# Kernel optimization log

Hardware: AMD Instinct MI355X
Metric: run time of the kernel (lower is better)

Reference implementation:

```python
import jax, jax.numpy as jnp
import numpy as np

N_LAYERS = 4
HID = 64
N_NODES = 50000
N_EDGES = 800000
N_GRAPHS = 256
NUM_ATOM = 100
NUM_BOND = 4
BN_EPS = 1e-5
GATE_EPS = 1e-6


def _batch_norm(x, gamma, beta):
    # training-mode BatchNorm1d over the node/edge dimension
    mu = jnp.mean(x, axis=0)
    var = jnp.var(x, axis=0)
    return gamma * (x - mu) * jax.lax.rsqrt(var + BN_EPS) + beta


def setup_inputs() -> dict:
    key = jax.random.key(0)
    ks = jax.random.split(key, 12)
    h = jax.random.randint(ks[0], (N_NODES,), 0, NUM_ATOM)
    e = jax.random.randint(ks[1], (N_EDGES,), 0, NUM_BOND)
    src = jax.random.randint(ks[2], (N_EDGES,), 0, N_NODES)
    dst = jax.random.randint(ks[3], (N_EDGES,), 0, N_NODES)
    graph_ids = jnp.sort(jax.random.randint(ks[4], (N_NODES,), 0, N_GRAPHS))
    node_emb = jax.random.normal(ks[5], (NUM_ATOM, HID), dtype=jnp.float32) * 0.1
    edge_emb = jax.random.normal(ks[6], (NUM_BOND, HID), dtype=jnp.float32) * 0.1
    bn_h_gamma = jnp.ones((N_LAYERS, HID), jnp.float32)
    bn_h_beta = jnp.zeros((N_LAYERS, HID), jnp.float32)
    bn_e_gamma = jnp.ones((N_LAYERS, HID), jnp.float32)
    bn_e_beta = jnp.zeros((N_LAYERS, HID), jnp.float32)
    W1 = jax.random.normal(ks[7], (HID, HID // 2), dtype=jnp.float32) * (1.0 / np.sqrt(HID))
    b1 = jnp.zeros((HID // 2,), jnp.float32)
    W2 = jax.random.normal(ks[8], (HID // 2, HID // 4), dtype=jnp.float32) * (1.0 / np.sqrt(HID // 2))
    b2 = jnp.zeros((HID // 4,), jnp.float32)
    W3 = jax.random.normal(ks[9], (HID // 4, 1), dtype=jnp.float32) * (1.0 / np.sqrt(HID // 4))
    b3 = jnp.zeros((1,), jnp.float32)
    return {"h": h, "e": e, "src": src, "dst": dst, "graph_ids": graph_ids,
            "node_emb": node_emb, "edge_emb": edge_emb,
            "bn_h_gamma": bn_h_gamma, "bn_h_beta": bn_h_beta,
            "bn_e_gamma": bn_e_gamma, "bn_e_beta": bn_e_beta,
            "W1": W1, "b1": b1, "W2": W2, "b2": b2, "W3": W3, "b3": b3}


def reference(h, e, src, dst, graph_ids, node_emb, edge_emb,
              bn_h_gamma, bn_h_beta, bn_e_gamma, bn_e_beta,
              W1, b1, W2, b2, W3, b3):
    hf = node_emb[h]          # [N, HID] node encoder
    ef = edge_emb[e]          # [E, HID] edge encoder
    ones_e = jnp.ones((N_EDGES,), hf.dtype)
    deg = jax.ops.segment_sum(ones_e, dst, num_segments=N_NODES)
    norm = jax.lax.rsqrt(jnp.maximum(deg, 1.0))[:, None]  # deg^-0.5, clamp(min=1)
    for l in range(N_LAYERS):
        h_in, e_in = hf, ef
        e_new = hf[src] + hf[dst] + ef            # gather: edge gate pre-activation
        sigma = jax.nn.sigmoid(e_new)
        hn = hf * norm
        msg = jax.ops.segment_sum(sigma * hn[src], dst, num_segments=N_NODES)
        den = jax.ops.segment_sum(sigma, dst, num_segments=N_NODES)
        h_new = (hn + msg / (den + GATE_EPS)) * norm
        h_new = _batch_norm(h_new, bn_h_gamma[l], bn_h_beta[l])
        e_new = _batch_norm(e_new, bn_e_gamma[l], bn_e_beta[l])
        hf = h_in + jax.nn.relu(h_new)            # residual
        ef = e_in + jax.nn.relu(e_new)
    # per-graph mean pooling (dgl.mean_nodes over the batched graph)
    ones_n = jnp.ones((N_NODES,), hf.dtype)
    counts = jax.ops.segment_sum(ones_n, graph_ids, num_segments=N_GRAPHS)
    hg = jax.ops.segment_sum(hf, graph_ids, num_segments=N_GRAPHS)
    hg = hg / jnp.maximum(counts, 1.0)[:, None]   # [G, HID]
    x = jax.nn.relu(hg @ W1 + b1)
    x = jax.nn.relu(x @ W2 + b2)
    return x @ W3 + b3                            # [G, 1]
```

## Files before the change

### kernel.cpp

```cpp
#include <hip/hip_runtime.h>
#include <math.h>

#define N_NODES 50000
#define N_EDGES 800000
#define HID 64
#define N_GRAPHS 256
#define BN_EPS 1e-5f
#define GATE_EPS 1e-6f

static inline size_t align256(size_t x) { return (x + 255) & ~(size_t)255; }


__global__ void k_zero(int* __restrict__ p, int n) {
    for (int i = blockIdx.x * blockDim.x + threadIdx.x; i < n; i += gridDim.x * blockDim.x)
        p[i] = 0;
}

__global__ void k_deg(const int* __restrict__ dst, int* __restrict__ deg) {
    for (int i = blockIdx.x * blockDim.x + threadIdx.x; i < N_EDGES; i += gridDim.x * blockDim.x)
        atomicAdd(&deg[dst[i]], 1);
}

__global__ void k_norm(const int* __restrict__ deg, float* __restrict__ norm) {
    int i = blockIdx.x * blockDim.x + threadIdx.x;
    if (i < N_NODES) norm[i] = 1.0f / sqrtf(fmaxf((float)deg[i], 1.0f));
}

__global__ void k_scan1(const int* __restrict__ deg, int* __restrict__ start,
                        int* __restrict__ blksum) {
    __shared__ int s[256];
    int t = threadIdx.x;
    int i = blockIdx.x * 256 + t;
    int v = (i < N_NODES) ? deg[i] : 0;
    s[t] = v;
    __syncthreads();
    for (int off = 1; off < 256; off <<= 1) {
        int x = (t >= off) ? s[t - off] : 0;
        __syncthreads();
        s[t] += x;
        __syncthreads();
    }
    if (i < N_NODES) start[i] = s[t] - v;
    if (t == 255) blksum[blockIdx.x] = s[255];
}

__global__ void k_scan2(int* __restrict__ blksum, int nb) {
    __shared__ int s[256];
    int t = threadIdx.x;
    int v = (t < nb) ? blksum[t] : 0;
    s[t] = v;
    __syncthreads();
    for (int off = 1; off < 256; off <<= 1) {
        int x = (t >= off) ? s[t - off] : 0;
        __syncthreads();
        s[t] += x;
        __syncthreads();
    }
    if (t < nb) blksum[t] = s[t] - v;
}

__global__ void k_scan3(int* __restrict__ start, const int* __restrict__ blksum,
                        int* __restrict__ cursor) {
    int i = blockIdx.x * 256 + threadIdx.x;
    if (i < N_NODES) {
        int v = start[i] + blksum[blockIdx.x];
        start[i] = v;
        cursor[i] = v;
    }
    if (blockIdx.x == 0 && threadIdx.x == 0) start[N_NODES] = N_EDGES;
}

__global__ void k_scatter(const int* __restrict__ dst, const int* __restrict__ src,
                          const int* __restrict__ etype, const float* __restrict__ norm,
                          int* __restrict__ cursor,
                          int* __restrict__ edge_pack, float* __restrict__ edge_norm) {
    for (int i = blockIdx.x * blockDim.x + threadIdx.x; i < N_EDGES; i += gridDim.x * blockDim.x) {
        int p = atomicAdd(&cursor[dst[i]], 1);
        int s = src[i];
        edge_pack[p] = s | (etype[i] << 24);
        edge_norm[p] = norm[s];
    }
}

__global__ __launch_bounds__(256) void k_embed(const int* __restrict__ h,
                                               const float* __restrict__ node_emb,
                                               float4* __restrict__ hf4) {
    const int total4 = N_NODES * (HID / 4);
    for (int i = blockIdx.x * blockDim.x + threadIdx.x; i < total4; i += gridDim.x * blockDim.x) {
        int n = i >> 4, c4 = i & 15;
        hf4[i] = ((const float4*)node_emb)[h[n] * (HID / 4) + c4];
    }
}

template <int MODE>
__global__ __launch_bounds__(256) void k_edge(
    const int* __restrict__ start, const int* __restrict__ edge_pack,
    const float* __restrict__ edge_norm, const float* __restrict__ edge_emb,
    float* __restrict__ ef,
    const float* __restrict__ hf_old, const float* __restrict__ hf_new,
    const float* __restrict__ norm, float* __restrict__ h_new,
    const float* __restrict__ stats_prev, const float* __restrict__ gamma_prev,
    const float* __restrict__ beta_prev,
    float* __restrict__ stats_e_out, float* __restrict__ stats_h_out) {
    const int lane = threadIdx.x & 63;
    const int gw = blockIdx.x * (blockDim.x >> 6) + (threadIdx.x >> 6);
    const int nw = gridDim.x * (blockDim.x >> 6);

    __shared__ float s_emb[4 * HID];
    if (MODE <= 1) {
        for (int i = threadIdx.x; i < 4 * HID; i += blockDim.x) s_emb[i] = edge_emb[i];
        __syncthreads();
    }
    float a_prev = 0.f, c_prev = 0.f;
    if (MODE >= 1) {
        float s1 = stats_prev[lane], s2 = stats_prev[HID + lane];
        float mu = s1 * (1.0f / N_EDGES);
        float var = s2 * (1.0f / N_EDGES) - mu * mu;
        float rstd = 1.0f / sqrtf(var + BN_EPS);
        a_prev = gamma_prev[lane] * rstd;
        c_prev = beta_prev[lane] - mu * a_prev;
    }

    float sum_e = 0.f, sumsq_e = 0.f, sum_h = 0.f, sumsq_h = 0.f;
    for (int n = gw; n < N_NODES; n += nw) {
        const int jbeg = start[n], jend = start[n + 1];
        const float h_new_n = hf_new[n * HID + lane];
        const float h_old_n = (MODE >= 1) ? hf_old[n * HID + lane] : 0.f;
        float amsg = 0.f, aden = 0.f;
        if (jbeg < jend) {
            int pk = edge_pack[jbeg];
            float ns = edge_norm[jbeg];
            int s = pk & 0xFFFFFF;
            float hs = hf_new[s * HID + lane];
            float ho = (MODE >= 1) ? hf_old[s * HID + lane] : 0.f;
            float efp = (MODE >= 2) ? ef[(size_t)jbeg * HID + lane] : 0.f;
            for (int j = jbeg; j < jend; ++j) {
                const int jn = (j + 1 < jend) ? j + 1 : jend - 1;
                const int pk_n = edge_pack[jn];
                const float ns_n = edge_norm[jn];
                const int s_n = pk_n & 0xFFFFFF;
                const float hs_n = hf_new[s_n * HID + lane];
                const float ho_n = (MODE >= 1) ? hf_old[s_n * HID + lane] : 0.f;
                const float efp_n = (MODE >= 2) ? ef[(size_t)jn * HID + lane] : 0.f;
                float efv;
                if (MODE == 0) {
                    efv = s_emb[(pk >> 24) * HID + lane];
                } else if (MODE == 1) {
                    const float ef0 = s_emb[(pk >> 24) * HID + lane];
                    const float ep = ho + h_old_n + ef0;
                    efv = ef0 + fmaxf(a_prev * ep + c_prev, 0.f);
                    ef[(size_t)j * HID + lane] = efv;
                } else {
                    const float ep = ho + h_old_n + efp;
                    efv = efp + fmaxf(a_prev * ep + c_prev, 0.f);
                    if (MODE == 2) ef[(size_t)j * HID + lane] = efv;
                }
                const float en = hs + h_new_n + efv;
                const float sg = 1.0f / (1.0f + __expf(-en));
                amsg += sg * hs * ns;
                aden += sg;
                if (MODE != 3) { sum_e += en; sumsq_e += en * en; }
                pk = pk_n; ns = ns_n; s = s_n; hs = hs_n; ho = ho_n; efp = efp_n;
            }
        }
        const float nm = norm[n];
        const float hval = (h_new_n * nm + amsg / (aden + GATE_EPS)) * nm;
        h_new[n * HID + lane] = hval;
        sum_h += hval;
        sumsq_h += hval * hval;
    }

    __shared__ float sred[4][256];
    sred[0][threadIdx.x] = sum_e;
    sred[1][threadIdx.x] = sumsq_e;
    sred[2][threadIdx.x] = sum_h;
    sred[3][threadIdx.x] = sumsq_h;
    __syncthreads();
    if (threadIdx.x < 64) {
        const int t = threadIdx.x;
        if (MODE != 3) {
            float t1 = sred[0][t] + sred[0][t + 64] + sred[0][t + 128] + sred[0][t + 192];
            float t2 = sred[1][t] + sred[1][t + 64] + sred[1][t + 128] + sred[1][t + 192];
            atomicAdd(&stats_e_out[t], t1);
            atomicAdd(&stats_e_out[HID + t], t2);
        }
        float t3 = sred[2][t] + sred[2][t + 64] + sred[2][t + 128] + sred[2][t + 192];
        float t4 = sred[3][t] + sred[3][t + 64] + sred[3][t + 128] + sred[3][t + 192];
        atomicAdd(&stats_h_out[t], t3);
        atomicAdd(&stats_h_out[HID + t], t4);
    }
}

__global__ __launch_bounds__(256) void k_hupd(
    const float4* __restrict__ hf_in, const float4* __restrict__ h_new,
    const float* __restrict__ stats, const float* __restrict__ gamma,
    const float* __restrict__ beta, float4* __restrict__ hf_out) {
    const int tid = blockIdx.x * blockDim.x + threadIdx.x;
    const int c0 = (tid & 15) * 4;
    float a[4], c[4];
#pragma unroll
    for (int k = 0; k < 4; ++k) {
        int ch = c0 + k;
        float mu = stats[ch] * (1.0f / N_NODES);
        float var = stats[HID + ch] * (1.0f / N_NODES) - mu * mu;
        float rstd = 1.0f / sqrtf(var + BN_EPS);
        a[k] = gamma[ch] * rstd;
        c[k] = beta[ch] - mu * a[k];
    }
    const int total4 = N_NODES * (HID / 4);
    for (int i = tid; i < total4; i += gridDim.x * blockDim.x) {
        float4 hi = hf_in[i], hn = h_new[i], o;
        o.x = hi.x + fmaxf(a[0] * hn.x + c[0], 0.f);
        o.y = hi.y + fmaxf(a[1] * hn.y + c[1], 0.f);
        o.z = hi.z + fmaxf(a[2] * hn.z + c[2], 0.f);
        o.w = hi.w + fmaxf(a[3] * hn.w + c[3], 0.f);
        hf_out[i] = o;
    }
}

__global__ __launch_bounds__(256) void k_poolmlp(
    const float* __restrict__ hf, const int* __restrict__ graph_ids,
    const float* __restrict__ W1, const float* __restrict__ b1,
    const float* __restrict__ W2, const float* __restrict__ b2,
    const float* __restrict__ W3, const float* __restrict__ b3,
    float* __restrict__ out) {
    const int g = blockIdx.x;
    int a = 0, b = N_NODES;
    while (a < b) { int m = (a + b) >> 1; if (graph_ids[m] < g) a = m + 1; else b = m; }
    const int lo = a;
    b = N_NODES;
    while (a < b) { int m = (a + b) >> 1; if (graph_ids[m] < g + 1) a = m + 1; else b = m; }
    const int hi = a;

    const int lane = threadIdx.x & 63, w = threadIdx.x >> 6;
    float acc = 0.f;
    for (int n = lo + w; n < hi; n += 4) acc += hf[n * HID + lane];
    __shared__ float sred[256];
    __shared__ float sh[64], sx1[32], sx2[16];
    sred[threadIdx.x] = acc;
    __syncthreads();
    if (threadIdx.x < 64) {
        float tot = sred[lane] + sred[lane + 64] + sred[lane + 128] + sred[lane + 192];
        sh[lane] = tot / fmaxf((float)(hi - lo), 1.0f);
    }
    __syncthreads();
    const int t = threadIdx.x;
    if (t < 32) {
        float s = b1[t];
        for (int c = 0; c < 64; ++c) s += sh[c] * W1[c * 32 + t];
        sx1[t] = fmaxf(s, 0.f);
    }
    __syncthreads();
    if (t < 16) {
        float s = b2[t];
        for (int k = 0; k < 32; ++k) s += sx1[k] * W2[k * 16 + t];
        sx2[t] = fmaxf(s, 0.f);
    }
    __syncthreads();
    if (t == 0) {
        float s = b3[0];
        for (int k = 0; k < 16; ++k) s += sx2[k] * W3[k];
        out[g] = s;
    }
}


extern "C" void kernel_launch(void* const* d_in, const int* in_sizes, int n_in,
                              void* d_out, int out_size, void* d_ws, size_t ws_size,
                              hipStream_t stream) {
    const int* h_idx      = (const int*)d_in[0];
    const int* e_idx      = (const int*)d_in[1];
    const int* src        = (const int*)d_in[2];
    const int* dst        = (const int*)d_in[3];
    const int* graph_ids  = (const int*)d_in[4];
    const float* node_emb = (const float*)d_in[5];
    const float* edge_emb = (const float*)d_in[6];
    const float* bnh_g    = (const float*)d_in[7];
    const float* bnh_b    = (const float*)d_in[8];
    const float* bne_g    = (const float*)d_in[9];
    const float* bne_b    = (const float*)d_in[10];
    const float* W1       = (const float*)d_in[11];
    const float* b1       = (const float*)d_in[12];
    const float* W2       = (const float*)d_in[13];
    const float* b2       = (const float*)d_in[14];
    const float* W3       = (const float*)d_in[15];
    const float* b3       = (const float*)d_in[16];
    float* out = (float*)d_out;

    char* w = (char*)d_ws;
    size_t off = 0;
    auto alloc = [&](size_t bytes) -> void* {
        void* p = w + off;
        off = align256(off + bytes);
        return p;
    };
    float* ef        = (float*)alloc((size_t)N_EDGES * HID * 4);
    float* hfA       = (float*)alloc((size_t)N_NODES * HID * 4);
    float* hfB       = (float*)alloc((size_t)N_NODES * HID * 4);
    float* h_new     = (float*)alloc((size_t)N_NODES * HID * 4);
    float* norm      = (float*)alloc((size_t)N_NODES * 4);
    int*   edge_pack = (int*)alloc((size_t)N_EDGES * 4);
    float* edge_norm = (float*)alloc((size_t)N_EDGES * 4);
    int*   start     = (int*)alloc((size_t)(N_NODES + 1) * 4);
    int*   cursor    = (int*)alloc((size_t)N_NODES * 4);
    int*   blksum    = (int*)alloc(256 * 4);
    size_t zoff = off;
    int*   deg       = (int*)alloc((size_t)N_NODES * 4);
    float* stats_e   = (float*)alloc(4 * 2 * HID * 4);
    float* stats_h   = (float*)alloc(4 * 2 * HID * 4);
    int zero_elems = (int)((off - zoff) / 4);
    int* zbase = (int*)(w + zoff);

    const int NB_SCAN = (N_NODES + 255) / 256;

    k_zero<<<64, 256, 0, stream>>>(zbase, zero_elems);
    k_deg<<<1024, 256, 0, stream>>>(dst, deg);
    k_norm<<<NB_SCAN, 256, 0, stream>>>(deg, norm);
    k_scan1<<<NB_SCAN, 256, 0, stream>>>(deg, start, blksum);
    k_scan2<<<1, 256, 0, stream>>>(blksum, NB_SCAN);
    k_scan3<<<NB_SCAN, 256, 0, stream>>>(start, blksum, cursor);
    k_scatter<<<1024, 256, 0, stream>>>(dst, src, e_idx, norm, cursor, edge_pack, edge_norm);
    k_embed<<<512, 256, 0, stream>>>(h_idx, node_emb, (float4*)hfA);

    const int EG = 2048;
    const int NG = 512;

    k_edge<0><<<EG, 256, 0, stream>>>(start, edge_pack, edge_norm, edge_emb, ef,
        nullptr, hfA, norm, h_new, nullptr, nullptr, nullptr,
        stats_e + 0 * 128, stats_h + 0 * 128);
    k_hupd<<<NG, 256, 0, stream>>>((const float4*)hfA, (const float4*)h_new,
        stats_h + 0 * 128, bnh_g + 0 * HID, bnh_b + 0 * HID, (float4*)hfB);

    k_edge<1><<<EG, 256, 0, stream>>>(start, edge_pack, edge_norm, edge_emb, ef,
        hfA, hfB, norm, h_new, stats_e + 0 * 128, bne_g + 0 * HID, bne_b + 0 * HID,
        stats_e + 1 * 128, stats_h + 1 * 128);
    k_hupd<<<NG, 256, 0, stream>>>((const float4*)hfB, (const float4*)h_new,
        stats_h + 1 * 128, bnh_g + 1 * HID, bnh_b + 1 * HID, (float4*)hfA);

    k_edge<2><<<EG, 256, 0, stream>>>(start, edge_pack, edge_norm, edge_emb, ef,
        hfB, hfA, norm, h_new, stats_e + 1 * 128, bne_g + 1 * HID, bne_b + 1 * HID,
        stats_e + 2 * 128, stats_h + 2 * 128);
    k_hupd<<<NG, 256, 0, stream>>>((const float4*)hfA, (const float4*)h_new,
        stats_h + 2 * 128, bnh_g + 2 * HID, bnh_b + 2 * HID, (float4*)hfB);

    k_edge<3><<<EG, 256, 0, stream>>>(start, edge_pack, edge_norm, edge_emb, ef,
        hfA, hfB, norm, h_new, stats_e + 2 * 128, bne_g + 2 * HID, bne_b + 2 * HID,
        stats_e + 3 * 128, stats_h + 3 * 128);
    k_hupd<<<NG, 256, 0, stream>>>((const float4*)hfB, (const float4*)h_new,
        stats_h + 3 * 128, bnh_g + 3 * HID, bnh_b + 3 * HID, (float4*)hfA);

    k_poolmlp<<<N_GRAPHS, 256, 0, stream>>>(hfA, graph_ids, W1, b1, W2, b2, W3, b3, out);
}
```

Measured before the change: 809.2 us.

## Interleave four destination nodes per wavefront and pack edge metadata into int2

Each wavefront now owns exactly four consecutive destination nodes and walks their incoming edge lists in lockstep, issuing four independent gathers per iteration instead of one chained software-prefetch stream. The grid grows to one wave per four nodes rather than a grid-stride loop. Source index, edge type and source norm are merged into a single int2 array, so each edge needs one 8-byte load instead of two separate loads. The aim is more memory-level parallelism on the latency-bound gathers. The cost is idle lanes and redundant clamped loads when the four nodes have unequal degrees, and the code relies on N_NODES being divisible by 16.

```diff
diff --git a/kernel.cpp b/kernel.cpp
--- a/kernel.cpp
+++ b/kernel.cpp
@@ -72,13 +72,11 @@
 
 __global__ void k_scatter(const int* __restrict__ dst, const int* __restrict__ src,
                           const int* __restrict__ etype, const float* __restrict__ norm,
-                          int* __restrict__ cursor,
-                          int* __restrict__ edge_pack, float* __restrict__ edge_norm) {
+                          int* __restrict__ cursor, int2* __restrict__ edge_meta) {
     for (int i = blockIdx.x * blockDim.x + threadIdx.x; i < N_EDGES; i += gridDim.x * blockDim.x) {
         int p = atomicAdd(&cursor[dst[i]], 1);
         int s = src[i];
-        edge_pack[p] = s | (etype[i] << 24);
-        edge_norm[p] = norm[s];
+        edge_meta[p] = make_int2(s | (etype[i] << 24), __float_as_int(norm[s]));
     }
 }
 
@@ -94,8 +92,8 @@
 
 template <int MODE>
 __global__ __launch_bounds__(256) void k_edge(
-    const int* __restrict__ start, const int* __restrict__ edge_pack,
-    const float* __restrict__ edge_norm, const float* __restrict__ edge_emb,
+    const int* __restrict__ start, const int2* __restrict__ edge_meta,
+    const float* __restrict__ edge_emb,
     float* __restrict__ ef,
     const float* __restrict__ hf_old, const float* __restrict__ hf_new,
     const float* __restrict__ norm, float* __restrict__ h_new,
@@ -103,8 +101,8 @@
     const float* __restrict__ beta_prev,
     float* __restrict__ stats_e_out, float* __restrict__ stats_h_out) {
     const int lane = threadIdx.x & 63;
-    const int gw = blockIdx.x * (blockDim.x >> 6) + (threadIdx.x >> 6);
-    const int nw = gridDim.x * (blockDim.x >> 6);
+    const int wid = __builtin_amdgcn_readfirstlane(blockIdx.x * 4 + (threadIdx.x >> 6));
+    const int n0 = wid * 4;
 
     __shared__ float s_emb[4 * HID];
     if (MODE <= 1) {
@@ -121,51 +119,60 @@
         c_prev = beta_prev[lane] - mu * a_prev;
     }
 
+    int jbeg[4], len[4];
+    float hnn[4], hon[4], amsg[4], aden[4];
+    int maxlen = 0;
+#pragma unroll
+    for (int k = 0; k < 4; ++k) {
+        jbeg[k] = start[n0 + k];
+        len[k] = start[n0 + k + 1] - jbeg[k];
+        maxlen = max(maxlen, len[k]);
+        hnn[k] = hf_new[(n0 + k) * HID + lane];
+        hon[k] = (MODE >= 1) ? hf_old[(n0 + k) * HID + lane] : 0.f;
+        amsg[k] = 0.f;
+        aden[k] = 0.f;
+    }
+
     float sum_e = 0.f, sumsq_e = 0.f, sum_h = 0.f, sumsq_h = 0.f;
-    for (int n = gw; n < N_NODES; n += nw) {
-        const int jbeg = start[n], jend = start[n + 1];
-        const float h_new_n = hf_new[n * HID + lane];
-        const float h_old_n = (MODE >= 1) ? hf_old[n * HID + lane] : 0.f;
-        float amsg = 0.f, aden = 0.f;
-        if (jbeg < jend) {
-            int pk = edge_pack[jbeg];
-            float ns = edge_norm[jbeg];
-            int s = pk & 0xFFFFFF;
-            float hs = hf_new[s * HID + lane];
-            float ho = (MODE >= 1) ? hf_old[s * HID + lane] : 0.f;
-            float efp = (MODE >= 2) ? ef[(size_t)jbeg * HID + lane] : 0.f;
-            for (int j = jbeg; j < jend; ++j) {
-                const int jn = (j + 1 < jend) ? j + 1 : jend - 1;
-                const int pk_n = edge_pack[jn];
-                const float ns_n = edge_norm[jn];
-                const int s_n = pk_n & 0xFFFFFF;
-                const float hs_n = hf_new[s_n * HID + lane];
-                const float ho_n = (MODE >= 1) ? hf_old[s_n * HID + lane] : 0.f;
-                const float efp_n = (MODE >= 2) ? ef[(size_t)jn * HID + lane] : 0.f;
-                float efv;
-                if (MODE == 0) {
-                    efv = s_emb[(pk >> 24) * HID + lane];
-                } else if (MODE == 1) {
-                    const float ef0 = s_emb[(pk >> 24) * HID + lane];
-                    const float ep = ho + h_old_n + ef0;
-                    efv = ef0 + fmaxf(a_prev * ep + c_prev, 0.f);
-                    ef[(size_t)j * HID + lane] = efv;
-                } else {
-                    const float ep = ho + h_old_n + efp;
-                    efv = efp + fmaxf(a_prev * ep + c_prev, 0.f);
-                    if (MODE == 2) ef[(size_t)j * HID + lane] = efv;
-                }
-                const float en = hs + h_new_n + efv;
-                const float sg = 1.0f / (1.0f + __expf(-en));
-                amsg += sg * hs * ns;
-                aden += sg;
+    for (int it = 0; it < maxlen; ++it) {
+#pragma unroll
+        for (int k = 0; k < 4; ++k) {
+            const bool act = it < len[k];
+            int jc = jbeg[k] + (act ? it : max(len[k] - 1, 0));
+            jc = min(jc, N_EDGES - 1);
+            const int2 mt = edge_meta[jc];
+            const int s = mt.x & 0xFFFFFF;
+            const float ns = __int_as_float(mt.y);
+            float efv;
+            if (MODE == 0) {
+                efv = s_emb[(mt.x >> 24) * HID + lane];
+            } else if (MODE == 1) {
+                const float ef0 = s_emb[(mt.x >> 24) * HID + lane];
+                const float ep = hf_old[s * HID + lane] + hon[k] + ef0;
+                efv = ef0 + fmaxf(a_prev * ep + c_prev, 0.f);
+                if (act) ef[(size_t)jc * HID + lane] = efv;
+            } else {
+                const float efp = ef[(size_t)jc * HID + lane];
+                const float ep = hf_old[s * HID + lane] + hon[k] + efp;
+                efv = efp + fmaxf(a_prev * ep + c_prev, 0.f);
+                if (MODE == 2) { if (act) ef[(size_t)jc * HID + lane] = efv; }
+            }
+            const float hs = hf_new[s * HID + lane];
+            const float en = hs + hnn[k] + efv;
+            const float sg = 1.0f / (1.0f + __expf(-en));
+            if (act) {
+                amsg[k] += sg * hs * ns;
+                aden[k] += sg;
                 if (MODE != 3) { sum_e += en; sumsq_e += en * en; }
-                pk = pk_n; ns = ns_n; s = s_n; hs = hs_n; ho = ho_n; efp = efp_n;
             }
         }
-        const float nm = norm[n];
-        const float hval = (h_new_n * nm + amsg / (aden + GATE_EPS)) * nm;
-        h_new[n * HID + lane] = hval;
+    }
+
+#pragma unroll
+    for (int k = 0; k < 4; ++k) {
+        const float nm = norm[n0 + k];
+        const float hval = (hnn[k] * nm + amsg[k] / (aden[k] + GATE_EPS)) * nm;
+        h_new[(n0 + k) * HID + lane] = hval;
         sum_h += hval;
         sumsq_h += hval * hval;
     }
@@ -299,8 +306,7 @@
     float* hfB       = (float*)alloc((size_t)N_NODES * HID * 4);
     float* h_new     = (float*)alloc((size_t)N_NODES * HID * 4);
     float* norm      = (float*)alloc((size_t)N_NODES * 4);
-    int*   edge_pack = (int*)alloc((size_t)N_EDGES * 4);
-    float* edge_norm = (float*)alloc((size_t)N_EDGES * 4);
+    int2*  edge_meta = (int2*)alloc((size_t)N_EDGES * 8);
     int*   start     = (int*)alloc((size_t)(N_NODES + 1) * 4);
     int*   cursor    = (int*)alloc((size_t)N_NODES * 4);
     int*   blksum    = (int*)alloc(256 * 4);
@@ -319,31 +325,31 @@
     k_scan1<<<NB_SCAN, 256, 0, stream>>>(deg, start, blksum);
     k_scan2<<<1, 256, 0, stream>>>(blksum, NB_SCAN);
     k_scan3<<<NB_SCAN, 256, 0, stream>>>(start, blksum, cursor);
-    k_scatter<<<1024, 256, 0, stream>>>(dst, src, e_idx, norm, cursor, edge_pack, edge_norm);
+    k_scatter<<<1024, 256, 0, stream>>>(dst, src, e_idx, norm, cursor, edge_meta);
     k_embed<<<512, 256, 0, stream>>>(h_idx, node_emb, (float4*)hfA);
 
-    const int EG = 2048;
+    const int EG = N_NODES / 16;
     const int NG = 512;
 
-    k_edge<0><<<EG, 256, 0, stream>>>(start, edge_pack, edge_norm, edge_emb, ef,
+    k_edge<0><<<EG, 256, 0, stream>>>(start, edge_meta, edge_emb, ef,
         nullptr, hfA, norm, h_new, nullptr, nullptr, nullptr,
         stats_e + 0 * 128, stats_h + 0 * 128);
     k_hupd<<<NG, 256, 0, stream>>>((const float4*)hfA, (const float4*)h_new,
         stats_h + 0 * 128, bnh_g + 0 * HID, bnh_b + 0 * HID, (float4*)hfB);
 
-    k_edge<1><<<EG, 256, 0, stream>>>(start, edge_pack, edge_norm, edge_emb, ef,
+    k_edge<1><<<EG, 256, 0, stream>>>(start, edge_meta, edge_emb, ef,
         hfA, hfB, norm, h_new, stats_e + 0 * 128, bne_g + 0 * HID, bne_b + 0 * HID,
         stats_e + 1 * 128, stats_h + 1 * 128);
     k_hupd<<<NG, 256, 0, stream>>>((const float4*)hfB, (const float4*)h_new,
         stats_h + 1 * 128, bnh_g + 1 * HID, bnh_b + 1 * HID, (float4*)hfA);
 
-    k_edge<2><<<EG, 256, 0, stream>>>(start, edge_pack, edge_norm, edge_emb, ef,
+    k_edge<2><<<EG, 256, 0, stream>>>(start, edge_meta, edge_emb, ef,
         hfB, hfA, norm, h_new, stats_e + 1 * 128, bne_g + 1 * HID, bne_b + 1 * HID,
         stats_e + 2 * 128, stats_h + 2 * 128);
     k_hupd<<<NG, 256, 0, stream>>>((const float4*)hfA, (const float4*)h_new,
         stats_h + 2 * 128, bnh_g + 2 * HID, bnh_b + 2 * HID, (float4*)hfB);
 
-    k_edge<3><<<EG, 256, 0, stream>>>(start, edge_pack, edge_norm, edge_emb, ef,
+    k_edge<3><<<EG, 256, 0, stream>>>(start, edge_meta, edge_emb, ef,
         hfA, hfB, norm, h_new, stats_e + 2 * 128, bne_g + 2 * HID, bne_b + 2 * HID,
         stats_e + 3 * 128, stats_h + 3 * 128);
     k_hupd<<<NG, 256, 0, stream>>>((const float4*)hfB, (const float4*)h_new,
```

Result: faster. 773.6 us (-4.4%).
